# Kernel tuning notes

Measured on AMD Instinct MI355X. Metric: run time of the kernel, lower is better.

Reference implementation:

```python
import math
import jax, jax.numpy as jnp
import numpy as np

# ---- config (mirrors ModelConfig) ----
B, T = 2, 2048
N_EMBD, N_HEAD, N_KV = 2048, 16, 4
DH = N_EMBD // N_HEAD          # 128
G = N_HEAD // N_KV             # 4
ROPE_THETA = 1e6
YARN_FACTOR = 64.0
ORIG_MAX_POS = 4096
BETA_FAST, BETA_SLOW = 4.0, 1.0
MSCALE, MSCALE_ALL_DIM = 1.0, 0.0


def _yarn_get_mscale(scale, mscale=1.0):
    if scale <= 1.0:
        return 1.0
    return 0.1 * mscale * math.log(scale) + 1.0


def yarn_inv_freq_and_factor():
    dim = DH
    base = ROPE_THETA
    factor = YARN_FACTOR
    if MSCALE and MSCALE_ALL_DIM:
        attn_factor = _yarn_get_mscale(factor, MSCALE) / _yarn_get_mscale(factor, MSCALE_ALL_DIM)
    else:
        attn_factor = _yarn_get_mscale(factor)

    def corr_dim(num_rot):
        return dim * math.log(ORIG_MAX_POS / (num_rot * 2 * math.pi)) / (2 * math.log(base))

    low = max(math.floor(corr_dim(BETA_FAST)), 0.0)
    high = min(math.ceil(corr_dim(BETA_SLOW)), float(dim - 1))
    if low == high:
        high += 0.001
    half = dim // 2
    t = np.arange(half, dtype=np.float32)
    ramp = np.clip((t - low) / (high - low), 0.0, 1.0)  # linear ramp
    pos = np.arange(0, dim, 2, dtype=np.float32) / dim
    pos_freqs = base ** pos
    inv_extrap = 1.0 / pos_freqs
    inv_interp = 1.0 / (factor * pos_freqs)
    extrap_factor = 1.0 - ramp
    inv = inv_interp * (1.0 - extrap_factor) + inv_extrap * extrap_factor
    return jnp.asarray(inv, jnp.float32), float(attn_factor)


INV_FREQ, ATTN_FACTOR = yarn_inv_freq_and_factor()


def apply_rope_yarn(x, positions, inv_freq, attn_factor):
    # x: [B, T, H, Dh] interleaved RoPE, then scale by attn_factor
    x32 = x.astype(jnp.float32)
    angles = positions.astype(jnp.float32)[:, None] * inv_freq[None, :]  # [T, Dh/2]
    cos = angles[None, :, None, :]  # broadcast shapes
    cos, sin = jnp.cos(cos), jnp.sin(angles)[None, :, None, :]
    x_even = x32[..., 0::2]
    x_odd = x32[..., 1::2]
    out_even = x_even * cos - x_odd * sin
    out_odd = x_even * sin + x_odd * cos
    out = jnp.stack([out_even, out_odd], axis=-1).reshape(x.shape)
    return (out * attn_factor).astype(x.dtype)


def setup_inputs() -> dict:
    key = jax.random.key(0)
    k1, k2, k3 = jax.random.split(key, 3)
    x = jax.random.normal(k1, (B, T, N_EMBD), jnp.float32)
    w_qkv = jax.random.normal(k2, (N_EMBD, N_EMBD + 2 * N_KV * DH), jnp.float32) * (N_EMBD ** -0.5)
    w_o = jax.random.normal(k3, (N_EMBD, N_EMBD), jnp.float32) * (N_EMBD ** -0.5)
    return {"x": x, "w_qkv": w_qkv, "w_o": w_o}


def reference(x, w_qkv, w_o):
    qkv = x @ w_qkv  # [B, T, n_embd + 2*n_kv*dh]
    q_raw = qkv[:, :, :N_EMBD]
    k_raw = qkv[:, :, N_EMBD:N_EMBD + N_KV * DH]
    v_raw = qkv[:, :, N_EMBD + N_KV * DH:]
    q = q_raw.reshape(B, T, N_HEAD, DH)
    k = k_raw.reshape(B, T, N_KV, DH)
    v = v_raw.reshape(B, T, N_KV, DH)

    pos = jnp.arange(T, dtype=jnp.int32)
    q = apply_rope_yarn(q, pos, INV_FREQ, ATTN_FACTOR)
    k = apply_rope_yarn(k, pos, INV_FREQ, ATTN_FACTOR)

    q = q.reshape(B, T, N_KV, G, DH).transpose(0, 2, 3, 1, 4)  # [B, kv, g, T, Dh]
    k = k.transpose(0, 2, 1, 3)  # [B, kv, T, Dh]
    v = v.transpose(0, 2, 1, 3)  # [B, kv, T, Dh]

    scale = 1.0 / math.sqrt(DH)
    att = jnp.einsum('bkgtd,bksd->bkgts', q, k) * scale
    causal = jnp.tril(jnp.ones((T, T), bool))[None, None, None]
    att = jnp.where(causal, att, jnp.asarray(-1e9, att.dtype))
    w = jax.nn.softmax(att, axis=-1)
    y = jnp.einsum('bkgts,bksd->bkgtd', w, v)
    y = y.transpose(0, 3, 1, 2, 4).reshape(B, T, N_EMBD)
    return y @ w_o
```

## Files before the change

kernel.cpp:

```cpp
#include <hip/hip_runtime.h>
#include <hip/hip_bf16.h>
#include <math.h>

#define B_    2
#define T_    2048
#define CEMB  2048
#define NH    16
#define NKV   4
#define DHD   128
#define QKVD  3072

typedef unsigned short u16;
typedef unsigned int   u32;
typedef __attribute__((ext_vector_type(8))) short  short8;
typedef __attribute__((ext_vector_type(4))) float  floatx4;

static __device__ __forceinline__ u16 f2bf(float f){
    union{float f;u32 u;}x; x.f = f; u32 u = x.u;
    return (u16)((u + 0x7fffu + ((u >> 16) & 1u)) >> 16);
}
static __device__ __forceinline__ float lo2f(u32 w){ union{u32 u;float f;}x; x.u = w << 16; return x.f; }
static __device__ __forceinline__ float hi2f(u32 w){ union{u32 u;float f;}x; x.u = w & 0xffff0000u; return x.f; }

static __device__ __forceinline__ u32 cvt_pk_bf16(float lo, float hi){
    u32 r;
    asm("v_cvt_pk_bf16_f32 %0, %1, %2" : "=v"(r) : "v"(lo), "v"(hi));
    return r;
}

static __device__ __forceinline__ void async_cp16(const u16* g, u16* lds_wave_base) {
    __builtin_amdgcn_global_load_lds(
        (const __attribute__((address_space(1))) void*)g,
        (__attribute__((address_space(3))) void*)lds_wave_base, 16, 0, 0);
}

__global__ __launch_bounds__(256) void convert_kernel(const float* __restrict__ in,
                                                      u16* __restrict__ out, int n8)
{
    const int i = blockIdx.x * 256 + threadIdx.x;
    if (i >= n8) return;
    const float4* p = reinterpret_cast<const float4*>(in);
    float4 a = p[i * 2], b = p[i * 2 + 1];
    uint4 o;
    o.x = (u32)f2bf(a.x) | ((u32)f2bf(a.y) << 16);
    o.y = (u32)f2bf(a.z) | ((u32)f2bf(a.w) << 16);
    o.z = (u32)f2bf(b.x) | ((u32)f2bf(b.y) << 16);
    o.w = (u32)f2bf(b.z) | ((u32)f2bf(b.w) << 16);
    reinterpret_cast<uint4*>(out)[i] = o;
}

__global__ __launch_bounds__(256) void transpose_f32_bf16(const float* __restrict__ in,
                                                          u16* __restrict__ out,
                                                          int R, int Cn)
{
    __shared__ float tl[32][33];
    const int tx = threadIdx.x & 31, ty = threadIdx.x >> 5;
    const int c0 = blockIdx.x << 5, r0 = blockIdx.y << 5;
    #pragma unroll
    for (int i = 0; i < 4; ++i)
        tl[ty + i * 8][tx] = in[(size_t)(r0 + ty + i * 8) * Cn + c0 + tx];
    __syncthreads();
    #pragma unroll
    for (int i = 0; i < 4; ++i)
        out[(size_t)(c0 + ty + i * 8) * R + r0 + tx] = f2bf(tl[tx][ty + i * 8]);
}

__global__ __launch_bounds__(256) void vt_build_kernel(const u16* __restrict__ qkv,
                                                       u16* __restrict__ vt)
{
    __shared__ u16 tl[32][33];
    const int tx = threadIdx.x & 31, ty = threadIdx.x >> 5;
    const int t0 = blockIdx.x << 5, d0 = blockIdx.y << 5;
    const int b = blockIdx.z >> 2, kv = blockIdx.z & 3;
    #pragma unroll
    for (int i = 0; i < 4; ++i)
        tl[ty + i * 8][tx] =
            qkv[(size_t)(b * T_ + t0 + ty + i * 8) * QKVD + CEMB + NKV * DHD + kv * DHD + d0 + tx];
    __syncthreads();
    #pragma unroll
    for (int i = 0; i < 4; ++i)
        vt[(size_t)((b * NKV + kv) * DHD + d0 + ty + i * 8) * T_ + t0 + tx] = tl[tx][ty + i * 8];
}

template <int BN_, int WM_, int WN_, bool F32OUT>
__global__ __launch_bounds__(512, 2) void gemm_mfma8_kernel(const u16* __restrict__ A,
                                                            const u16* __restrict__ BT,
                                                            void* __restrict__ Cv,
                                                            int M, int N, int K)
{
    constexpr int BM = 256, BK = 64;
    constexpr int MR = BM / WM_ / 16;
    constexpr int NR = BN_ / WN_ / 16;
    constexpr int AR = (BM * BK * 2) / 8192;
    constexpr int BR = (BN_ * BK * 2) / 8192;
    constexpr int LPT = AR + BR;

    __shared__ __align__(16) u16 As[2][BM * BK];
    __shared__ __align__(16) u16 Bs[2][BN_ * BK];

    const int tid  = threadIdx.x;
    const int lane = tid & 63;
    const int wv   = tid >> 6;
    const int n16  = lane & 15;
    const int quad = lane >> 4;
    const int wm   = wv / WN_;
    const int wn   = wv % WN_;

    const int GX  = gridDim.x;
    const int nwg = GX * gridDim.y;
    const int lin = blockIdx.y * GX + blockIdx.x;
    const int swz = (lin & 7) * (nwg >> 3) + (lin >> 3);
    const int row0 = (swz / GX) * BM;
    const int col0 = (swz % GX) * BN_;

    auto stage = [&](int t, int buf) {
        const int k0 = t * BK;
        const int rA = tid >> 3;
        const int lc = (tid & 7) ^ (rA & 7);
        #pragma unroll
        for (int r = 0; r < AR; ++r)
            async_cp16(A + (size_t)(row0 + r * 64 + rA) * K + k0 + (lc << 3),
                       &As[buf][(r * 512 + wv * 64) * 8]);
        #pragma unroll
        for (int r = 0; r < BR; ++r)
            async_cp16(BT + (size_t)(col0 + r * 64 + rA) * K + k0 + (lc << 3),
                       &Bs[buf][(r * 512 + wv * 64) * 8]);
    };

    floatx4 acc[MR][NR];
    #pragma unroll
    for (int m = 0; m < MR; ++m)
        #pragma unroll
        for (int n = 0; n < NR; ++n) acc[m][n] = (floatx4)0.0f;

    const int nt = K / BK;
    stage(0, 0);
    stage(1, 1);

    for (int t = 0; t < nt; ++t) {
        const int cur = t & 1;
        if (t + 1 < nt) asm volatile("s_waitcnt vmcnt(%0)" :: "i"(LPT) : "memory");
        else            asm volatile("s_waitcnt vmcnt(0)" ::: "memory");
        __builtin_amdgcn_s_barrier();

        const u16* as = As[cur];
        const u16* bs = Bs[cur];
        #pragma unroll
        for (int kh = 0; kh < 2; ++kh) {
            short8 af[MR], bf[NR];
            #pragma unroll
            for (int m = 0; m < MR; ++m) {
                const int row = wm * (BM / WM_) + m * 16 + n16;
                af[m] = *reinterpret_cast<const short8*>(
                    &as[row * BK + (((kh * 4 + quad) ^ (row & 7)) << 3)]);
            }
            #pragma unroll
            for (int n = 0; n < NR; ++n) {
                const int col = wn * (BN_ / WN_) + n * 16 + n16;
                bf[n] = *reinterpret_cast<const short8*>(
                    &bs[col * BK + (((kh * 4 + quad) ^ (col & 7)) << 3)]);
            }
            __builtin_amdgcn_s_setprio(1);
            #pragma unroll
            for (int m = 0; m < MR; ++m)
                #pragma unroll
                for (int n = 0; n < NR; ++n)
                    acc[m][n] = __builtin_amdgcn_mfma_f32_16x16x32_bf16(af[m], bf[n], acc[m][n], 0, 0, 0);
            __builtin_amdgcn_s_setprio(0);
        }

        asm volatile("s_waitcnt lgkmcnt(0)" ::: "memory");
        __builtin_amdgcn_s_barrier();
        __builtin_amdgcn_sched_barrier(0);
        if (t + 2 < nt) stage(t + 2, cur);
    }

    #pragma unroll
    for (int m = 0; m < MR; ++m) {
        #pragma unroll
        for (int r = 0; r < 4; ++r) {
            const int row = row0 + wm * (BM / WM_) + m * 16 + quad * 4 + r;
            if (F32OUT) {
                float* C = reinterpret_cast<float*>(Cv);
                #pragma unroll
                for (int n = 0; n < NR; ++n)
                    C[(size_t)row * N + col0 + wn * (BN_ / WN_) + n * 16 + n16] = acc[m][n][r];
            } else {
                u16* C = reinterpret_cast<u16*>(Cv);
                #pragma unroll
                for (int n = 0; n < NR; ++n)
                    C[(size_t)row * N + col0 + wn * (BN_ / WN_) + n * 16 + n16] = f2bf(acc[m][n][r]);
            }
        }
    }
}

__global__ __launch_bounds__(256) void rope_kernel(
    u16* __restrict__ qkv, const float attn_factor, const float low, const float high)
{
    const int total = B_ * T_ * (NH + NKV) * (DHD / 2);
    int idx = blockIdx.x * 256 + threadIdx.x;
    if (idx >= total) return;
    const int d = idx & 63;
    int r = idx >> 6;
    const int h = r % (NH + NKV);
    r /= (NH + NKV);
    const int t = r % T_;
    const int b = r / T_;
    const int off = (h < NH) ? (h * DHD) : (CEMB + (h - NH) * DHD);

    u32* p = reinterpret_cast<u32*>(qkv + (size_t)(b * T_ + t) * QKVD + off) + d;
    u32 w = *p;
    float xe = lo2f(w), xo = hi2f(w);

    float df   = (float)d;
    float ramp = (df - low) / (high - low);
    ramp = fminf(fmaxf(ramp, 0.0f), 1.0f);
    float pf     = expf((2.0f * df / 128.0f) * 13.815510557964274f);
    float inv_ex = 1.0f / pf;
    float inv    = inv_ex * ((1.0f / 64.0f) * ramp + (1.0f - ramp));
    float ang = (float)t * inv;
    float s = sinf(ang), c = cosf(ang);
    float oe = (xe * c - xo * s) * attn_factor;
    float oo = (xe * s + xo * c) * attn_factor;
    *p = (u32)f2bf(oe) | ((u32)f2bf(oo) << 16);
}

__global__ __launch_bounds__(512, 4) void attn_mfma_kernel(const u16* __restrict__ qkv,
                                                           const u16* __restrict__ vt,
                                                           u16* __restrict__ y)
{
    __shared__ __align__(16) u16 Ksd[2][64 * 128];
    __shared__ __align__(16) u16 Vtsd[2][128 * 64];
    __shared__ __align__(16) u16 Pl[8 * 1024];

    const int tid  = threadIdx.x;
    const int lane = tid & 63;
    const int wv   = tid >> 6;
    const int n16  = lane & 15;
    const int quad = lane >> 4;

    const int lin = blockIdx.y * 16 + blockIdx.x;
    const int swz = (lin & 7) * 64 + (lin >> 3);
    const int nx  = swz & 15;
    const int bh  = swz >> 4;
    const int b   = bh >> 4;
    const int h   = bh & 15;
    const int kh  = h >> 2;

    const float C1 = 0.08838834764831845f * 1.4426950408889634f;

    u16* plw = Pl + wv * 1024;
    const int psw = (n16 & 7) << 3;

    const u16* kbase = qkv + (size_t)(b * T_) * QKVD + CEMB + kh * DHD;
    const u16* vbase = vt + (size_t)((b * NKV + kh) * DHD) * T_;

    auto dma_k = [&](int j0, int buf) {
        #pragma unroll
        for (int it = 0; it < 2; ++it) {
            const int P   = it * 512 + tid;
            const int row = P >> 4;
            const int lc  = (P & 15) ^ (row & 15);
            async_cp16(kbase + (size_t)(j0 + row) * QKVD + (lc << 3),
                       &Ksd[buf][(it * 512 + wv * 64) * 8]);
        }
    };
    auto dma_v = [&](int j0, int buf) {
        #pragma unroll
        for (int it = 0; it < 2; ++it) {
            const int P   = it * 512 + tid;
            const int row = P >> 3;
            const int lc  = (P & 7) ^ (row & 7);
            async_cp16(vbase + (size_t)row * T_ + j0 + (lc << 3),
                       &Vtsd[buf][(it * 512 + wv * 64) * 8]);
        }
    };

    const int i0H = (31 - nx) << 6;
    const int i0  = (wv < 4) ? i0H : (nx << 6);
    const int qb  = i0 + (wv & 3) * 16;
    const int qrow = qb + n16;

    const u16* qp = qkv + (size_t)(b * T_ + qrow) * QKVD + h * DHD;
    short8 qf[4];
    #pragma unroll
    for (int kk = 0; kk < 4; ++kk)
        qf[kk] = *reinterpret_cast<const short8*>(qp + kk * 32 + quad * 8);

    floatx4 oacc[8];
    #pragma unroll
    for (int i = 0; i < 8; ++i) oacc[i] = (floatx4)0.0f;
    float m_cur = -INFINITY, l_cur = 0.0f;

    dma_k(0, 0);
    dma_v(0, 0);

    for (int j0 = 0; j0 <= i0H; j0 += 64) {
        const int buf = (j0 >> 6) & 1;
        __syncthreads();
        if (j0 + 64 <= i0H) {
            dma_k(j0 + 64, buf ^ 1);
            dma_v(j0 + 64, buf ^ 1);
        }
        if (j0 > i0) continue;

        const u16* kb = Ksd[buf];
        const u16* vb = Vtsd[buf];

        floatx4 st[4];
        #pragma unroll
        for (int t = 0; t < 4; ++t) st[t] = (floatx4)0.0f;
        __builtin_amdgcn_s_setprio(1);
        #pragma unroll
        for (int t = 0; t < 4; ++t) {
            #pragma unroll
            for (int kk = 0; kk < 4; ++kk) {
                short8 a = *reinterpret_cast<const short8*>(
                    &kb[(t * 16 + n16) * 128 + (((kk * 4 + quad) ^ n16) << 3)]);
                st[t] = __builtin_amdgcn_mfma_f32_16x16x32_bf16(a, qf[kk], st[t], 0, 0, 0);
            }
        }
        __builtin_amdgcn_s_setprio(0);

        const bool diag = (j0 + 63 > qb);
        float tmax = -INFINITY;
        #pragma unroll
        for (int t = 0; t < 4; ++t) {
            if (diag) {
                #pragma unroll
                for (int r = 0; r < 4; ++r) {
                    const int key = j0 + t * 16 + quad * 4 + r;
                    if (key > qrow) st[t][r] = -INFINITY;
                }
            }
            tmax = fmaxf(tmax,
                         fmaxf(fmaxf(st[t][0], st[t][1]), fmaxf(st[t][2], st[t][3])));
        }
        tmax = fmaxf(tmax, __shfl_xor(tmax, 16));
        tmax = fmaxf(tmax, __shfl_xor(tmax, 32));

        if (!__all((tmax - m_cur) * C1 <= 8.0f)) {
            const float mnew  = fmaxf(m_cur, tmax);
            const float alpha = exp2f((m_cur - mnew) * C1);
            m_cur = mnew;
            l_cur *= alpha;
            #pragma unroll
            for (int dt = 0; dt < 8; ++dt) {
                oacc[dt][0] *= alpha; oacc[dt][1] *= alpha;
                oacc[dt][2] *= alpha; oacc[dt][3] *= alpha;
            }
        }

        const float mC = m_cur * C1;
        float lsum = 0.0f;
        #pragma unroll
        for (int t = 0; t < 4; ++t) {
            float p0 = exp2f(fmaf(st[t][0], C1, -mC));
            float p1 = exp2f(fmaf(st[t][1], C1, -mC));
            float p2 = exp2f(fmaf(st[t][2], C1, -mC));
            float p3 = exp2f(fmaf(st[t][3], C1, -mC));
            lsum += (p0 + p1) + (p2 + p3);
            uint2 pk;
            pk.x = cvt_pk_bf16(p0, p1);
            pk.y = cvt_pk_bf16(p2, p3);
            *reinterpret_cast<uint2*>(&plw[n16 * 64 + ((t * 16 + quad * 4) ^ psw)]) = pk;
        }
        lsum += __shfl_xor(lsum, 16);
        lsum += __shfl_xor(lsum, 32);
        l_cur += lsum;

        __builtin_amdgcn_s_setprio(1);
        #pragma unroll
        for (int kt = 0; kt < 2; ++kt) {
            short8 pfrag = *reinterpret_cast<const short8*>(
                &plw[n16 * 64 + ((kt * 32 + quad * 8) ^ psw)]);
            #pragma unroll
            for (int dt = 0; dt < 8; ++dt) {
                short8 vfrag = *reinterpret_cast<const short8*>(
                    &vb[(dt * 16 + n16) * 64 + (((kt * 4 + quad) ^ (n16 & 7)) << 3)]);
                oacc[dt] = __builtin_amdgcn_mfma_f32_16x16x32_bf16(vfrag, pfrag, oacc[dt], 0, 0, 0);
            }
        }
        __builtin_amdgcn_s_setprio(0);
    }

    const float linv = 1.0f / l_cur;
    u16* yp = y + (size_t)(b * T_ + qrow) * CEMB + h * DHD + quad * 4;
    #pragma unroll
    for (int dt = 0; dt < 8; ++dt) {
        float a0 = oacc[dt][0] * linv, a1 = oacc[dt][1] * linv;
        float a2 = oacc[dt][2] * linv, a3 = oacc[dt][3] * linv;
        u32 w0 = cvt_pk_bf16(a0, a1);
        u32 w1 = cvt_pk_bf16(a2, a3);
        *reinterpret_cast<u32*>(yp + dt * 16)     = w0;
        *reinterpret_cast<u32*>(yp + dt * 16 + 2) = w1;
    }
}

extern "C" void kernel_launch(void* const* d_in, const int* in_sizes, int n_in,
                              void* d_out, int out_size, void* d_ws, size_t ws_size,
                              hipStream_t stream) {
    const size_t NX   = (size_t)B_ * T_ * CEMB;
    const size_t NWQ  = (size_t)CEMB * QKVD;
    const size_t NWO  = (size_t)CEMB * CEMB;
    const size_t NQKV = (size_t)B_ * T_ * QKVD;
    const size_t NY   = NX;

    u16* qkv = (u16*)d_ws;
    u16* y   = qkv + NQKV;
    u16* xb  = y + NY;
    u16* wqT = xb + NX;
    u16* woT = wqT + NWQ;
    u16* vtb = xb;

    convert_kernel<<<(int)(NX / 8 + 255) / 256, 256, 0, stream>>>((const float*)d_in[0], xb, (int)(NX / 8));
    transpose_f32_bf16<<<dim3(QKVD / 32, CEMB / 32), 256, 0, stream>>>((const float*)d_in[1], wqT, CEMB, QKVD);
    transpose_f32_bf16<<<dim3(CEMB / 32, CEMB / 32), 256, 0, stream>>>((const float*)d_in[2], woT, CEMB, CEMB);

    gemm_mfma8_kernel<192, 2, 4, false><<<dim3(QKVD / 192, (B_ * T_) / 256), 512, 0, stream>>>(
        xb, wqT, qkv, B_ * T_, QKVD, CEMB);

    const double two_pi = 6.283185307179586476925286766559;
    double corr4 = 128.0 * log(4096.0 / (4.0 * two_pi)) / (2.0 * log(1.0e6));
    double corr1 = 128.0 * log(4096.0 / (1.0 * two_pi)) / (2.0 * log(1.0e6));
    double lowd  = floor(corr4); if (lowd < 0.0) lowd = 0.0;
    double highd = ceil(corr1);  if (highd > 127.0) highd = 127.0;
    if (lowd == highd) highd += 0.001;
    float attn_factor = (float)(0.1 * log(64.0) + 1.0);

    const int rope_total = B_ * T_ * (NH + NKV) * (DHD / 2);
    rope_kernel<<<(rope_total + 255) / 256, 256, 0, stream>>>(
        qkv, attn_factor, (float)lowd, (float)highd);

    vt_build_kernel<<<dim3(T_ / 32, DHD / 32, B_ * NKV), 256, 0, stream>>>(qkv, vtb);

    attn_mfma_kernel<<<dim3(T_ / 128, B_ * NH), 512, 0, stream>>>(qkv, vtb, y);

    gemm_mfma8_kernel<128, 4, 2, true><<<dim3(CEMB / 128, (B_ * T_) / 256), 512, 0, stream>>>(
        y, woT, d_out, B_ * T_, CEMB, CEMB);
}
```

Measured before the change: 299.3 us.

## Interleave async tile loads with MFMA phases in a finer-grained GEMM pipeline

Replaces the GEMM main loop with a four-phase schedule. Each k-tile is split into sub-steps by M-half and K-half, and the global-to-LDS copies for the next tile are issued between the LDS reads and MFMAs of the current one. Staged vmcnt waits and barriers replace the old single wait per tile. The warp layout changes to 2x4 for both GEMMs, and loads are now double-buffered one tile ahead instead of two. The aim is to hide global load latency and LDS traffic behind matrix math, at the cost of more barriers and hand-tuned wait counts that must stay correct.

```diff
diff --git a/kernel.cpp b/kernel.cpp
--- a/kernel.cpp
+++ b/kernel.cpp
@@ -82,18 +82,19 @@
         vt[(size_t)((b * NKV + kv) * DHD + d0 + ty + i * 8) * T_ + t0 + tx] = tl[tx][ty + i * 8];
 }
 
-template <int BN_, int WM_, int WN_, bool F32OUT>
-__global__ __launch_bounds__(512, 2) void gemm_mfma8_kernel(const u16* __restrict__ A,
-                                                            const u16* __restrict__ BT,
-                                                            void* __restrict__ Cv,
-                                                            int M, int N, int K)
-{
-    constexpr int BM = 256, BK = 64;
-    constexpr int MR = BM / WM_ / 16;
-    constexpr int NR = BN_ / WN_ / 16;
-    constexpr int AR = (BM * BK * 2) / 8192;
-    constexpr int BR = (BN_ * BK * 2) / 8192;
-    constexpr int LPT = AR + BR;
+template <int BN_, bool F32OUT>
+__global__ __launch_bounds__(512, 2) void gemm_pipe_kernel(const u16* __restrict__ A,
+                                                           const u16* __restrict__ BT,
+                                                           void* __restrict__ Cv,
+                                                           int M, int N, int K)
+{
+    constexpr int BM  = 256, BK = 64;
+    constexpr int NR  = BN_ / 4 / 16;
+    constexpr int NBC = BN_ / 64;
+    constexpr int W1  = (BN_ == 192) ? 5 : 4;
+    constexpr int W2  = (BN_ == 192) ? 5 : 4;
+    constexpr int W3  = (BN_ == 192) ? 7 : 6;
+    constexpr int W4  = 2;
 
     __shared__ __align__(16) u16 As[2][BM * BK];
     __shared__ __align__(16) u16 Bs[2][BN_ * BK];
@@ -103,8 +104,8 @@
     const int wv   = tid >> 6;
     const int n16  = lane & 15;
     const int quad = lane >> 4;
-    const int wm   = wv / WN_;
-    const int wn   = wv % WN_;
+    const int wm   = wv >> 2;
+    const int wn   = wv & 3;
 
     const int GX  = gridDim.x;
     const int nwg = GX * gridDim.y;
@@ -113,83 +114,114 @@
     const int row0 = (swz / GX) * BM;
     const int col0 = (swz % GX) * BN_;
 
-    auto stage = [&](int t, int buf) {
+    auto stageA = [&](int t, int buf, int half) {
         const int k0 = t * BK;
         const int rA = tid >> 3;
         const int lc = (tid & 7) ^ (rA & 7);
         #pragma unroll
-        for (int r = 0; r < AR; ++r)
-            async_cp16(A + (size_t)(row0 + r * 64 + rA) * K + k0 + (lc << 3),
-                       &As[buf][(r * 512 + wv * 64) * 8]);
-        #pragma unroll
-        for (int r = 0; r < BR; ++r)
-            async_cp16(BT + (size_t)(col0 + r * 64 + rA) * K + k0 + (lc << 3),
-                       &Bs[buf][(r * 512 + wv * 64) * 8]);
-    };
-
-    floatx4 acc[MR][NR];
-    #pragma unroll
-    for (int m = 0; m < MR; ++m)
+        for (int r = 0; r < 2; ++r)
+            async_cp16(A + (size_t)(row0 + half * 128 + r * 64 + rA) * K + k0 + (lc << 3),
+                       &As[buf][((half * 2 + r) * 512 + wv * 64) * 8]);
+    };
+    auto stageB = [&](int t, int buf, int c) {
+        const int k0 = t * BK;
+        const int rA = tid >> 3;
+        const int lc = (tid & 7) ^ (rA & 7);
+        async_cp16(BT + (size_t)(col0 + c * 64 + rA) * K + k0 + (lc << 3),
+                   &Bs[buf][(c * 512 + wv * 64) * 8]);
+    };
+
+    floatx4 acc[8][NR];
+    #pragma unroll
+    for (int m = 0; m < 8; ++m)
         #pragma unroll
         for (int n = 0; n < NR; ++n) acc[m][n] = (floatx4)0.0f;
 
+    auto rd = [&](short8* af, short8* bf, int mh, int kh, int cur) {
+        const u16* as = As[cur];
+        const u16* bs = Bs[cur];
+        #pragma unroll
+        for (int mf = 0; mf < 4; ++mf) {
+            const int row = wm * 128 + mh * 64 + mf * 16 + n16;
+            af[mf] = *reinterpret_cast<const short8*>(
+                &as[row * 64 + (((kh * 4 + quad) ^ (row & 7)) << 3)]);
+        }
+        #pragma unroll
+        for (int nf = 0; nf < NR; ++nf) {
+            const int col = wn * (BN_ / 4) + nf * 16 + n16;
+            bf[nf] = *reinterpret_cast<const short8*>(
+                &bs[col * 64 + (((kh * 4 + quad) ^ (col & 7)) << 3)]);
+        }
+    };
+    auto mm = [&](short8* af, short8* bf, int mh) {
+        asm volatile("s_waitcnt lgkmcnt(0)" ::: "memory");
+        __builtin_amdgcn_sched_barrier(0);
+        __builtin_amdgcn_s_setprio(1);
+        #pragma unroll
+        for (int mf = 0; mf < 4; ++mf)
+            #pragma unroll
+            for (int nf = 0; nf < NR; ++nf)
+                acc[mh * 4 + mf][nf] =
+                    __builtin_amdgcn_mfma_f32_16x16x32_bf16(af[mf], bf[nf], acc[mh * 4 + mf][nf], 0, 0, 0);
+        __builtin_amdgcn_s_setprio(0);
+    };
+
     const int nt = K / BK;
-    stage(0, 0);
-    stage(1, 1);
+
+    #pragma unroll
+    for (int c = 0; c < NBC; ++c) stageB(0, 0, c);
+    stageA(0, 0, 0);
+    stageA(0, 0, 1);
+    asm volatile("s_waitcnt vmcnt(2)" ::: "memory");
+    asm volatile("s_barrier" ::: "memory");
 
     for (int t = 0; t < nt; ++t) {
         const int cur = t & 1;
-        if (t + 1 < nt) asm volatile("s_waitcnt vmcnt(%0)" :: "i"(LPT) : "memory");
-        else            asm volatile("s_waitcnt vmcnt(0)" ::: "memory");
-        __builtin_amdgcn_s_barrier();
-
-        const u16* as = As[cur];
-        const u16* bs = Bs[cur];
-        #pragma unroll
-        for (int kh = 0; kh < 2; ++kh) {
-            short8 af[MR], bf[NR];
-            #pragma unroll
-            for (int m = 0; m < MR; ++m) {
-                const int row = wm * (BM / WM_) + m * 16 + n16;
-                af[m] = *reinterpret_cast<const short8*>(
-                    &as[row * BK + (((kh * 4 + quad) ^ (row & 7)) << 3)]);
-            }
-            #pragma unroll
-            for (int n = 0; n < NR; ++n) {
-                const int col = wn * (BN_ / WN_) + n * 16 + n16;
-                bf[n] = *reinterpret_cast<const short8*>(
-                    &bs[col * BK + (((kh * 4 + quad) ^ (col & 7)) << 3)]);
-            }
-            __builtin_amdgcn_s_setprio(1);
-            #pragma unroll
-            for (int m = 0; m < MR; ++m)
-                #pragma unroll
-                for (int n = 0; n < NR; ++n)
-                    acc[m][n] = __builtin_amdgcn_mfma_f32_16x16x32_bf16(af[m], bf[n], acc[m][n], 0, 0, 0);
-            __builtin_amdgcn_s_setprio(0);
-        }
-
-        asm volatile("s_waitcnt lgkmcnt(0)" ::: "memory");
-        __builtin_amdgcn_s_barrier();
-        __builtin_amdgcn_sched_barrier(0);
-        if (t + 2 < nt) stage(t + 2, cur);
+        const int w   = (t + 1 < nt) ? (t + 1) : t;
+        const int wb  = (t + 1) & 1;
+        short8 af[4], bf[NR];
+
+        rd(af, bf, 0, 0, cur);
+        #pragma unroll
+        for (int c = 0; c < NBC; ++c) stageB(w, wb, c);
+        mm(af, bf, 0);
+        asm volatile("s_waitcnt vmcnt(%0)" :: "i"(W1) : "memory");
+        asm volatile("s_barrier" ::: "memory");
+
+        rd(af, bf, 0, 1, cur);
+        stageA(w, wb, 0);
+        mm(af, bf, 0);
+        asm volatile("s_waitcnt vmcnt(%0)" :: "i"(W2) : "memory");
+        asm volatile("s_barrier" ::: "memory");
+
+        rd(af, bf, 1, 0, cur);
+        stageA(w, wb, 1);
+        mm(af, bf, 1);
+        asm volatile("s_waitcnt vmcnt(%0)" :: "i"(W3) : "memory");
+        asm volatile("s_barrier" ::: "memory");
+
+        rd(af, bf, 1, 1, cur);
+        mm(af, bf, 1);
+        asm volatile("s_waitcnt vmcnt(%0)" :: "i"(W4) : "memory");
+        asm volatile("s_barrier" ::: "memory");
     }
-
-    #pragma unroll
-    for (int m = 0; m < MR; ++m) {
+    asm volatile("s_waitcnt vmcnt(0)" ::: "memory");
+
+    #pragma unroll
+    for (int mi = 0; mi < 8; ++mi) {
         #pragma unroll
         for (int r = 0; r < 4; ++r) {
-            const int row = row0 + wm * (BM / WM_) + m * 16 + quad * 4 + r;
+            const int row = row0 + wm * 128 + (mi >> 2) * 64 + (mi & 3) * 16 + quad * 4 + r;
             if (F32OUT) {
                 float* C = reinterpret_cast<float*>(Cv);
                 #pragma unroll
-                for (int n = 0; n < NR; ++n)
-                    C[(size_t)row * N + col0 + wn * (BN_ / WN_) + n * 16 + n16] = acc[m][n][r];
+                for (int nf = 0; nf < NR; ++nf)
+                    C[(size_t)row * N + col0 + wn * (BN_ / 4) + nf * 16 + n16] = acc[mi][nf][r];
             } else {
                 u16* C = reinterpret_cast<u16*>(Cv);
                 #pragma unroll
-                for (int n = 0; n < NR; ++n)
-                    C[(size_t)row * N + col0 + wn * (BN_ / WN_) + n * 16 + n16] = f2bf(acc[m][n][r]);
+                for (int nf = 0; nf < NR; ++nf)
+                    C[(size_t)row * N + col0 + wn * (BN_ / 4) + nf * 16 + n16] = f2bf(acc[mi][nf][r]);
             }
         }
     }
@@ -418,7 +450,7 @@
     transpose_f32_bf16<<<dim3(QKVD / 32, CEMB / 32), 256, 0, stream>>>((const float*)d_in[1], wqT, CEMB, QKVD);
     transpose_f32_bf16<<<dim3(CEMB / 32, CEMB / 32), 256, 0, stream>>>((const float*)d_in[2], woT, CEMB, CEMB);
 
-    gemm_mfma8_kernel<192, 2, 4, false><<<dim3(QKVD / 192, (B_ * T_) / 256), 512, 0, stream>>>(
+    gemm_pipe_kernel<192, false><<<dim3(QKVD / 192, (B_ * T_) / 256), 512, 0, stream>>>(
         xb, wqT, qkv, B_ * T_, QKVD, CEMB);
 
     const double two_pi = 6.283185307179586476925286766559;
@@ -437,6 +469,6 @@
 
     attn_mfma_kernel<<<dim3(T_ / 128, B_ * NH), 512, 0, stream>>>(qkv, vtb, y);
 
-    gemm_mfma8_kernel<128, 4, 2, true><<<dim3(CEMB / 128, (B_ * T_) / 256), 512, 0, stream>>>(
+    gemm_pipe_kernel<128, true><<<dim3(CEMB / 128, (B_ * T_) / 256), 512, 0, stream>>>(
         y, woT, d_out, B_ * T_, CEMB, CEMB);
 }
```

Result: slower. 309.0 us (+3.2%).
